# Optimization experiments

Hardware: AMD Instinct MI355X
Metric: run time of the kernel (lower is better)

## Reference

```python
import jax, jax.numpy as jnp
import numpy as np

SEQ, BATCH, HID = 4096, 32, 512

def setup_inputs() -> dict:
    key = jax.random.key(0)
    k1, k2, k3, k4 = jax.random.split(key, 4)
    stdv = 1.0 / np.sqrt(HID)
    x = jax.random.normal(k1, (SEQ, BATCH, HID), dtype=jnp.float32)
    W = jax.random.uniform(k2, (HID, HID), dtype=jnp.float32, minval=-stdv, maxval=stdv)
    b = jax.random.uniform(k3, (HID,), dtype=jnp.float32, minval=-stdv, maxval=stdv)
    context = jax.random.uniform(k4, (HID,), dtype=jnp.float32, minval=-stdv, maxval=stdv)
    return {"x": x, "W": W, "b": b, "context": context}

def reference(x, W, b, context):
    # x: [seq, batch, hid] -> [batch, seq, hid]
    xb = jnp.transpose(x, (1, 0, 2))
    # tanh(Linear(x)) per timestep, batched as one GEMM
    attends = jnp.tanh(jnp.einsum('bsh,oh->bso', xb, W) + b)
    # additive-attention scores via dot with context vector -> [batch, seq]
    similarity = jnp.einsum('bsh,h->bs', attends, context)
    probs = jax.nn.softmax(similarity, axis=-1)  # softmax over seq
    # weighted-sum pooling -> [batch, hid]
    attended = jnp.einsum('bsh,bs->bh', xb, probs)
    return attended
```

## Files before the change

### kernel.cpp

```cpp
#include <hip/hip_runtime.h>
#include <hip/hip_bf16.h>

#define SEQ   4096
#define BATCH 32
#define HID   512
#define MTOT  (SEQ * BATCH)

typedef float  f32x4  __attribute__((ext_vector_type(4)));
typedef __bf16 bf16x8 __attribute__((ext_vector_type(8)));
typedef unsigned short ushort8v __attribute__((ext_vector_type(8)));
typedef unsigned int u32;

__device__ __forceinline__ unsigned short f2bf(float f) {
    unsigned int u = __builtin_bit_cast(unsigned int, f);
    u = (u + 0x7fffu + ((u >> 16) & 1u)) >> 16;
    return (unsigned short)u;
}

__device__ __forceinline__ float tanh_fast(float x) {
    float ax = fabsf(x);
    float e  = __expf(-2.0f * ax);
    float t  = (1.0f - e) * __builtin_amdgcn_rcpf(1.0f + e);
    return copysignf(t, x);
}

__device__ __forceinline__ void g2l16(const void* g, void* l) {
    __builtin_amdgcn_global_load_lds(
        (const __attribute__((address_space(1))) u32*)g,
        (__attribute__((address_space(3))) u32*)l, 16, 0, 0);
}

__global__ __launch_bounds__(256) void cvt_w_kernel(const float* __restrict__ W,
                                                    unsigned short* __restrict__ Wb) {
    int i = (blockIdx.x * 256 + threadIdx.x) * 4;
    float4 f = *(const float4*)(W + i);
    ushort4 u;
    u.x = f2bf(f.x); u.y = f2bf(f.y); u.z = f2bf(f.z); u.w = f2bf(f.w);
    *(ushort4*)(Wb + i) = u;
}

__global__ __launch_bounds__(256) void cvt_x_kernel(const float* __restrict__ x,
                                                    unsigned short* __restrict__ xb) {
    size_t i = ((size_t)blockIdx.x * 256 + threadIdx.x) * 8;
    float4 a0 = *(const float4*)(x + i);
    float4 a1 = *(const float4*)(x + i + 4);
    ushort8v v;
    v[0] = f2bf(a0.x); v[1] = f2bf(a0.y); v[2] = f2bf(a0.z); v[3] = f2bf(a0.w);
    v[4] = f2bf(a1.x); v[5] = f2bf(a1.y); v[6] = f2bf(a1.z); v[7] = f2bf(a1.w);
    *(ushort8v*)(xb + i) = v;
}

__global__ __launch_bounds__(256) void gemm_sim_bf16(
    const unsigned short* __restrict__ xb, const unsigned short* __restrict__ Wb,
    const float* __restrict__ bias, const float* __restrict__ ctx,
    float* __restrict__ simsT)
{
    __shared__ __align__(16) unsigned short As[128 * 64];
    __shared__ __align__(16) unsigned short Bs[128 * 64];

    const int L    = blockIdx.x;
    const int xcd  = L & 7;
    const int slot = L >> 3;
    const int nt   = slot & 3;
    const int mt   = xcd * 128 + (slot >> 2);

    const int tid  = threadIdx.x;
    const int lane = tid & 63;
    const int wave = tid >> 6;
    const int wm = wave >> 1, wn = wave & 1;
    const int l15 = lane & 15, q = lane >> 4;

    const int srow  = lane >> 3;
    const int skoff = ((lane & 7) ^ srow) * 8;

    const unsigned short* Abase = xb + (size_t)(mt * 128) * HID;
    const unsigned short* Bbase = Wb + (size_t)(nt * 128) * HID;

    f32x4 acc[4][4] = {};

    for (int kt = 0; kt < HID / 64; ++kt) {
        const int k0 = kt * 64;
        #pragma unroll
        for (int t = 0; t < 4; ++t) {
            const int c = wave * 4 + t;
            g2l16(Abase + (size_t)(c * 8 + srow) * HID + k0 + skoff, &As[c * 512]);
            g2l16(Bbase + (size_t)(c * 8 + srow) * HID + k0 + skoff, &Bs[c * 512]);
        }
        __syncthreads();
        #pragma unroll
        for (int kh = 0; kh < 2; ++kh) {
            bf16x8 af[4], bfr[4];
            const int lc = kh * 4 + q;
            #pragma unroll
            for (int mi = 0; mi < 4; ++mi) {
                const int row = wm * 64 + mi * 16 + l15;
                af[mi] = *(const bf16x8*)&As[row * 64 + (lc ^ (row & 7)) * 8];
            }
            #pragma unroll
            for (int ni = 0; ni < 4; ++ni) {
                const int row = wn * 64 + ni * 16 + l15;
                bfr[ni] = *(const bf16x8*)&Bs[row * 64 + (lc ^ (row & 7)) * 8];
            }
            #pragma unroll
            for (int mi = 0; mi < 4; ++mi)
                #pragma unroll
                for (int ni = 0; ni < 4; ++ni)
                    acc[mi][ni] = __builtin_amdgcn_mfma_f32_16x16x32_bf16(
                        af[mi], bfr[ni], acc[mi][ni], 0, 0, 0);
        }
        __syncthreads();
    }

    float ps[16];
    #pragma unroll
    for (int mi = 0; mi < 4; ++mi)
        #pragma unroll
        for (int r = 0; r < 4; ++r) {
            float s = 0.f;
            #pragma unroll
            for (int ni = 0; ni < 4; ++ni) {
                const int o = nt * 128 + wn * 64 + ni * 16 + l15;
                float y = acc[mi][ni][r] + bias[o];
                s += ctx[o] * tanh_fast(y);
            }
            ps[mi * 4 + r] = s;
        }
    #pragma unroll
    for (int off = 1; off < 16; off <<= 1)
        #pragma unroll
        for (int i = 0; i < 16; ++i)
            ps[i] += __shfl_xor(ps[i], off, 64);
    if (l15 == 0) {
        float* dst = simsT + (size_t)(nt * 2 + wn) * MTOT;
        #pragma unroll
        for (int mi = 0; mi < 4; ++mi)
            #pragma unroll
            for (int r = 0; r < 4; ++r) {
                const int m = mt * 128 + wm * 64 + mi * 16 + q * 4 + r;
                dst[(m & 31) * SEQ + (m >> 5)] = ps[mi * 4 + r];
            }
    }
}

#define LDSP 72
__global__ __launch_bounds__(256) void gemm_sim_f32(
    const float* __restrict__ x, const unsigned short* __restrict__ Wb,
    const float* __restrict__ bias, const float* __restrict__ ctx,
    float* __restrict__ simsT)
{
    __shared__ __align__(16) unsigned short As[128][LDSP];
    __shared__ __align__(16) unsigned short Bs[128][LDSP];

    const int L    = blockIdx.x;
    const int xcd  = L & 7;
    const int slot = L >> 3;
    const int nt   = slot & 3;
    const int mt   = xcd * 128 + (slot >> 2);

    const int tid  = threadIdx.x;
    const int lane = tid & 63;
    const int wave = tid >> 6;
    const int wm = wave >> 1, wn = wave & 1;
    const int l15 = lane & 15, q = lane >> 4;
    const int rbase = tid >> 3;
    const int kc    = (tid & 7) * 8;

    f32x4 acc[4][4] = {};
    for (int kt = 0; kt < HID / 64; ++kt) {
        const int k0 = kt * 64;
        #pragma unroll
        for (int j = 0; j < 4; ++j) {
            const int row = rbase + j * 32;
            const float4* asrc = (const float4*)(x + (size_t)(mt * 128 + row) * HID + k0 + kc);
            float4 a0 = asrc[0];
            float4 a1 = asrc[1];
            uint4 bsrc = *(const uint4*)(Wb + (size_t)(nt * 128 + row) * HID + k0 + kc);
            ushort8v v;
            v[0] = f2bf(a0.x); v[1] = f2bf(a0.y); v[2] = f2bf(a0.z); v[3] = f2bf(a0.w);
            v[4] = f2bf(a1.x); v[5] = f2bf(a1.y); v[6] = f2bf(a1.z); v[7] = f2bf(a1.w);
            *(ushort8v*)&As[row][kc] = v;
            *(uint4*)&Bs[row][kc]    = bsrc;
        }
        __syncthreads();
        #pragma unroll
        for (int kh = 0; kh < 2; ++kh) {
            bf16x8 af[4], bfr[4];
            #pragma unroll
            for (int mi = 0; mi < 4; ++mi)
                af[mi] = *(const bf16x8*)&As[wm * 64 + mi * 16 + l15][kh * 32 + q * 8];
            #pragma unroll
            for (int ni = 0; ni < 4; ++ni)
                bfr[ni] = *(const bf16x8*)&Bs[wn * 64 + ni * 16 + l15][kh * 32 + q * 8];
            #pragma unroll
            for (int mi = 0; mi < 4; ++mi)
                #pragma unroll
                for (int ni = 0; ni < 4; ++ni)
                    acc[mi][ni] = __builtin_amdgcn_mfma_f32_16x16x32_bf16(
                        af[mi], bfr[ni], acc[mi][ni], 0, 0, 0);
        }
        __syncthreads();
    }
    float ps[16];
    #pragma unroll
    for (int mi = 0; mi < 4; ++mi)
        #pragma unroll
        for (int r = 0; r < 4; ++r) {
            float s = 0.f;
            #pragma unroll
            for (int ni = 0; ni < 4; ++ni) {
                const int o = nt * 128 + wn * 64 + ni * 16 + l15;
                s += ctx[o] * tanh_fast(acc[mi][ni][r] + bias[o]);
            }
            ps[mi * 4 + r] = s;
        }
    #pragma unroll
    for (int off = 1; off < 16; off <<= 1)
        #pragma unroll
        for (int i = 0; i < 16; ++i)
            ps[i] += __shfl_xor(ps[i], off, 64);
    if (l15 == 0) {
        float* dst = simsT + (size_t)(nt * 2 + wn) * MTOT;
        #pragma unroll
        for (int mi = 0; mi < 4; ++mi)
            #pragma unroll
            for (int r = 0; r < 4; ++r) {
                const int m = mt * 128 + wm * 64 + mi * 16 + q * 4 + r;
                dst[(m & 31) * SEQ + (m >> 5)] = ps[mi * 4 + r];
            }
    }
}

__global__ __launch_bounds__(256) void softmax_kernel(const float* __restrict__ simsT,
                                                      float* __restrict__ probsT) {
    const int b = blockIdx.x;
    const int tid = threadIdx.x;
    const int lane = tid & 63, wave = tid >> 6;
    __shared__ float red[4];

    float v[16];
    #pragma unroll
    for (int i = 0; i < 16; ++i) {
        const int s = i * 256 + tid;
        float acc = 0.f;
        #pragma unroll
        for (int p = 0; p < 8; ++p)
            acc += simsT[(size_t)p * MTOT + b * SEQ + s];
        v[i] = acc;
    }

    float mx = -INFINITY;
    #pragma unroll
    for (int i = 0; i < 16; ++i) mx = fmaxf(mx, v[i]);
    #pragma unroll
    for (int off = 32; off >= 1; off >>= 1) mx = fmaxf(mx, __shfl_xor(mx, off, 64));
    if (lane == 0) red[wave] = mx;
    __syncthreads();
    mx = fmaxf(fmaxf(red[0], red[1]), fmaxf(red[2], red[3]));
    __syncthreads();

    float sum = 0.f;
    #pragma unroll
    for (int i = 0; i < 16; ++i) { v[i] = __expf(v[i] - mx); sum += v[i]; }
    #pragma unroll
    for (int off = 32; off >= 1; off >>= 1) sum += __shfl_xor(sum, off, 64);
    if (lane == 0) red[wave] = sum;
    __syncthreads();
    const float inv = 1.0f / (red[0] + red[1] + red[2] + red[3]);

    #pragma unroll
    for (int i = 0; i < 16; ++i)
        probsT[b * SEQ + i * 256 + tid] = v[i] * inv;
}

__global__ __launch_bounds__(128) void attend_kernel(const float* __restrict__ x,
                                                     const float* __restrict__ probsT,
                                                     float* __restrict__ out) {
    const int st  = blockIdx.x;
    const int b   = blockIdx.y;
    const int tid = threadIdx.x;
    __shared__ float p[128];
    p[tid] = probsT[b * SEQ + st * 128 + tid];
    __syncthreads();
    f32x4 acc = {};
    const f32x4* xp = (const f32x4*)x + ((size_t)st * 128 * BATCH + b) * (HID / 4) + tid;
    #pragma unroll 8
    for (int s = 0; s < 128; ++s)
        acc += p[s] * xp[(size_t)s * (BATCH * HID / 4)];
    float* o = out + b * HID + tid * 4;
    atomicAdd(o + 0, acc[0]);
    atomicAdd(o + 1, acc[1]);
    atomicAdd(o + 2, acc[2]);
    atomicAdd(o + 3, acc[3]);
}

extern "C" void kernel_launch(void* const* d_in, const int* in_sizes, int n_in,
                              void* d_out, int out_size, void* d_ws, size_t ws_size,
                              hipStream_t stream) {
    const float* x    = (const float*)d_in[0];
    const float* W    = (const float*)d_in[1];
    const float* bias = (const float*)d_in[2];
    const float* ctx  = (const float*)d_in[3];
    float* out = (float*)d_out;

    const size_t xb_bytes    = (size_t)MTOT * HID * 2;
    const size_t wb_bytes    = (size_t)HID * HID * 2;
    const size_t sims_bytes  = (size_t)8 * MTOT * 4;
    const size_t probs_bytes = (size_t)MTOT * 4;
    const bool big = ws_size >= xb_bytes + wb_bytes + sims_bytes + probs_bytes;

    char* w = (char*)d_ws;
    unsigned short* xb = (unsigned short*)w;
    unsigned short* Wb;
    float *simsT, *probsT;
    if (big) {
        Wb     = (unsigned short*)(w + xb_bytes);
        simsT  = (float*)(w + xb_bytes + wb_bytes);
        probsT = (float*)(w + xb_bytes + wb_bytes + sims_bytes);
    } else {
        Wb     = (unsigned short*)w;
        simsT  = (float*)(w + wb_bytes);
        probsT = (float*)(w + wb_bytes + sims_bytes);
    }

    hipMemsetAsync(d_out, 0, (size_t)out_size * sizeof(float), stream);
    cvt_w_kernel<<<HID * HID / 1024, 256, 0, stream>>>(W, Wb);
    if (big) {
        cvt_x_kernel<<<(int)((size_t)MTOT * HID / 2048), 256, 0, stream>>>(x, xb);
        gemm_sim_bf16<<<4096, 256, 0, stream>>>(xb, Wb, bias, ctx, simsT);
    } else {
        gemm_sim_f32<<<4096, 256, 0, stream>>>(x, Wb, bias, ctx, simsT);
    }
    softmax_kernel<<<BATCH, 256, 0, stream>>>(simsT, probsT);
    attend_kernel<<<dim3(32, 32), 128, 0, stream>>>(x, probsT, out);
}
```

Measured before the change: 557.2 us.

## Fuse x bf16 conversion into GEMM load path, drop separate cvt_x pass

```diff
diff --git a/kernel.cpp b/kernel.cpp
--- a/kernel.cpp
+++ b/kernel.cpp
@@ -7,8 +7,8 @@
 #define MTOT  (SEQ * BATCH)
 
 typedef float  f32x4  __attribute__((ext_vector_type(4)));
+typedef float  f32x8  __attribute__((ext_vector_type(8)));
 typedef __bf16 bf16x8 __attribute__((ext_vector_type(8)));
-typedef unsigned short ushort8v __attribute__((ext_vector_type(8)));
 typedef unsigned int u32;
 
 __device__ __forceinline__ unsigned short f2bf(float f) {
@@ -39,19 +39,8 @@
     *(ushort4*)(Wb + i) = u;
 }
 
-__global__ __launch_bounds__(256) void cvt_x_kernel(const float* __restrict__ x,
-                                                    unsigned short* __restrict__ xb) {
-    size_t i = ((size_t)blockIdx.x * 256 + threadIdx.x) * 8;
-    float4 a0 = *(const float4*)(x + i);
-    float4 a1 = *(const float4*)(x + i + 4);
-    ushort8v v;
-    v[0] = f2bf(a0.x); v[1] = f2bf(a0.y); v[2] = f2bf(a0.z); v[3] = f2bf(a0.w);
-    v[4] = f2bf(a1.x); v[5] = f2bf(a1.y); v[6] = f2bf(a1.z); v[7] = f2bf(a1.w);
-    *(ushort8v*)(xb + i) = v;
-}
-
-__global__ __launch_bounds__(256) void gemm_sim_bf16(
-    const unsigned short* __restrict__ xb, const unsigned short* __restrict__ Wb,
+__global__ __launch_bounds__(256) void gemm_sim_kernel(
+    const float* __restrict__ x, const unsigned short* __restrict__ Wb,
     const float* __restrict__ bias, const float* __restrict__ ctx,
     float* __restrict__ simsT)
 {
@@ -72,8 +61,11 @@
 
     const int srow  = lane >> 3;
     const int skoff = ((lane & 7) ^ srow) * 8;
-
-    const unsigned short* Abase = xb + (size_t)(mt * 128) * HID;
+    const int arow = tid >> 3;
+    const int ac   = tid & 7;
+    const int apc  = ac ^ (arow & 7);
+
+    const float*          Abase = x  + (size_t)(mt * 128) * HID;
     const unsigned short* Bbase = Wb + (size_t)(nt * 128) * HID;
 
     f32x4 acc[4][4] = {};
@@ -83,8 +75,17 @@
         #pragma unroll
         for (int t = 0; t < 4; ++t) {
             const int c = wave * 4 + t;
-            g2l16(Abase + (size_t)(c * 8 + srow) * HID + k0 + skoff, &As[c * 512]);
             g2l16(Bbase + (size_t)(c * 8 + srow) * HID + k0 + skoff, &Bs[c * 512]);
+        }
+        #pragma unroll
+        for (int j = 0; j < 4; ++j) {
+            const int row = arow + j * 32;
+            const float4* asrc = (const float4*)(Abase + (size_t)row * HID + k0 + ac * 8);
+            float4 a0 = asrc[0];
+            float4 a1 = asrc[1];
+            f32x8 f = {a0.x, a0.y, a0.z, a0.w, a1.x, a1.y, a1.z, a1.w};
+            bf16x8 v = __builtin_convertvector(f, bf16x8);
+            *(bf16x8*)&As[row * 64 + apc * 8] = v;
         }
         __syncthreads();
         #pragma unroll
@@ -111,95 +112,6 @@
         __syncthreads();
     }
 
-    float ps[16];
-    #pragma unroll
-    for (int mi = 0; mi < 4; ++mi)
-        #pragma unroll
-        for (int r = 0; r < 4; ++r) {
-            float s = 0.f;
-            #pragma unroll
-            for (int ni = 0; ni < 4; ++ni) {
-                const int o = nt * 128 + wn * 64 + ni * 16 + l15;
-                float y = acc[mi][ni][r] + bias[o];
-                s += ctx[o] * tanh_fast(y);
-            }
-            ps[mi * 4 + r] = s;
-        }
-    #pragma unroll
-    for (int off = 1; off < 16; off <<= 1)
-        #pragma unroll
-        for (int i = 0; i < 16; ++i)
-            ps[i] += __shfl_xor(ps[i], off, 64);
-    if (l15 == 0) {
-        float* dst = simsT + (size_t)(nt * 2 + wn) * MTOT;
-        #pragma unroll
-        for (int mi = 0; mi < 4; ++mi)
-            #pragma unroll
-            for (int r = 0; r < 4; ++r) {
-                const int m = mt * 128 + wm * 64 + mi * 16 + q * 4 + r;
-                dst[(m & 31) * SEQ + (m >> 5)] = ps[mi * 4 + r];
-            }
-    }
-}
-
-#define LDSP 72
-__global__ __launch_bounds__(256) void gemm_sim_f32(
-    const float* __restrict__ x, const unsigned short* __restrict__ Wb,
-    const float* __restrict__ bias, const float* __restrict__ ctx,
-    float* __restrict__ simsT)
-{
-    __shared__ __align__(16) unsigned short As[128][LDSP];
-    __shared__ __align__(16) unsigned short Bs[128][LDSP];
-
-    const int L    = blockIdx.x;
-    const int xcd  = L & 7;
-    const int slot = L >> 3;
-    const int nt   = slot & 3;
-    const int mt   = xcd * 128 + (slot >> 2);
-
-    const int tid  = threadIdx.x;
-    const int lane = tid & 63;
-    const int wave = tid >> 6;
-    const int wm = wave >> 1, wn = wave & 1;
-    const int l15 = lane & 15, q = lane >> 4;
-    const int rbase = tid >> 3;
-    const int kc    = (tid & 7) * 8;
-
-    f32x4 acc[4][4] = {};
-    for (int kt = 0; kt < HID / 64; ++kt) {
-        const int k0 = kt * 64;
-        #pragma unroll
-        for (int j = 0; j < 4; ++j) {
-            const int row = rbase + j * 32;
-            const float4* asrc = (const float4*)(x + (size_t)(mt * 128 + row) * HID + k0 + kc);
-            float4 a0 = asrc[0];
-            float4 a1 = asrc[1];
-            uint4 bsrc = *(const uint4*)(Wb + (size_t)(nt * 128 + row) * HID + k0 + kc);
-            ushort8v v;
-            v[0] = f2bf(a0.x); v[1] = f2bf(a0.y); v[2] = f2bf(a0.z); v[3] = f2bf(a0.w);
-            v[4] = f2bf(a1.x); v[5] = f2bf(a1.y); v[6] = f2bf(a1.z); v[7] = f2bf(a1.w);
-            *(ushort8v*)&As[row][kc] = v;
-            *(uint4*)&Bs[row][kc]    = bsrc;
-        }
-        __syncthreads();
-        #pragma unroll
-        for (int kh = 0; kh < 2; ++kh) {
-            bf16x8 af[4], bfr[4];
-            #pragma unroll
-            for (int mi = 0; mi < 4; ++mi)
-                af[mi] = *(const bf16x8*)&As[wm * 64 + mi * 16 + l15][kh * 32 + q * 8];
-            #pragma unroll
-            for (int ni = 0; ni < 4; ++ni)
-                bfr[ni] = *(const bf16x8*)&Bs[wn * 64 + ni * 16 + l15][kh * 32 + q * 8];
-            #pragma unroll
-            for (int mi = 0; mi < 4; ++mi)
-                #pragma unroll
-                for (int ni = 0; ni < 4; ++ni)
-                    acc[mi][ni] = __builtin_amdgcn_mfma_f32_16x16x32_bf16(
-                        af[mi], bfr[ni], acc[mi][ni], 0, 0, 0);
-        }
-        __syncthreads();
-    }
     float ps[16];
     #pragma unroll
     for (int mi = 0; mi < 4; ++mi)
@@ -302,34 +214,14 @@
     const float* ctx  = (const float*)d_in[3];
     float* out = (float*)d_out;
 
-    const size_t xb_bytes    = (size_t)MTOT * HID * 2;
-    const size_t wb_bytes    = (size_t)HID * HID * 2;
-    const size_t sims_bytes  = (size_t)8 * MTOT * 4;
-    const size_t probs_bytes = (size_t)MTOT * 4;
-    const bool big = ws_size >= xb_bytes + wb_bytes + sims_bytes + probs_bytes;
-
     char* w = (char*)d_ws;
-    unsigned short* xb = (unsigned short*)w;
-    unsigned short* Wb;
-    float *simsT, *probsT;
-    if (big) {
-        Wb     = (unsigned short*)(w + xb_bytes);
-        simsT  = (float*)(w + xb_bytes + wb_bytes);
-        probsT = (float*)(w + xb_bytes + wb_bytes + sims_bytes);
-    } else {
-        Wb     = (unsigned short*)w;
-        simsT  = (float*)(w + wb_bytes);
-        probsT = (float*)(w + wb_bytes + sims_bytes);
-    }
+    unsigned short* Wb     = (unsigned short*)w;
+    float*          simsT  = (float*)(w + (512 << 10));
+    float*          probsT = (float*)(w + (512 << 10) + (4 << 20));
 
     hipMemsetAsync(d_out, 0, (size_t)out_size * sizeof(float), stream);
     cvt_w_kernel<<<HID * HID / 1024, 256, 0, stream>>>(W, Wb);
-    if (big) {
-        cvt_x_kernel<<<(int)((size_t)MTOT * HID / 2048), 256, 0, stream>>>(x, xb);
-        gemm_sim_bf16<<<4096, 256, 0, stream>>>(xb, Wb, bias, ctx, simsT);
-    } else {
-        gemm_sim_f32<<<4096, 256, 0, stream>>>(x, Wb, bias, ctx, simsT);
-    }
+    gemm_sim_kernel<<<4096, 256, 0, stream>>>(x, Wb, bias, ctx, simsT);
     softmax_kernel<<<BATCH, 256, 0, stream>>>(simsT, probsT);
     attend_kernel<<<dim3(32, 32), 128, 0, stream>>>(x, probsT, out);
 }
```

After: 496.8 us. 1.12x faster.
